# Kernel tuning notes

Measured on AMD Instinct MI355X. Metric: run time of the kernel, lower is better.

The kernel has to match this reference:

```python
import jax, jax.numpy as jnp
import numpy as np
import math

LMAX = 2
MUL = 50          # hidden multiplicity
NB = 10           # number_of_basis (hard-coded in module)
MAXR = 4.0        # max_radius
NLAYERS = 3
NUM_NEIGH = 2.0
E_EDGES = 40000
N_NODES = 2 * E_EDGES
SL = {0: slice(0, 1), 1: slice(1, 4), 2: slice(4, 9)}  # l=0,1,2 slices of the 9-dim multiplet
PATHS = [(0,0,0),(0,1,1),(0,2,2),(1,0,1),(1,1,0),(1,1,1),(1,1,2),
         (1,2,1),(1,2,2),(2,0,2),(2,1,1),(2,1,2),(2,2,0),(2,2,1),(2,2,2)]
NPATH_IN = {0: 3.0, 1: 6.0, 2: 6.0}  # number of TP paths feeding each output l

# ---- e3nn component-normalized real spherical harmonics up to l=2 (numpy, for CG setup) ----
def _sh_np(v):
    x, y, z = v[:, 0], v[:, 1], v[:, 2]
    s3, s5, s15 = 3**0.5, 5**0.5, 15**0.5
    return np.stack([np.ones_like(x), s3*x, s3*y, s3*z,
                     s15*x*z, s15*x*y, s5*(y*y - 0.5*(x*x + z*z)),
                     s15*y*z, (s15/2)*(z*z - x*x)], axis=1)

# ---- numerically derive the (unit-norm) Wigner-3j coupling tensors consistent with _sh_np ----
def _compute_w3j():
    rng = np.random.default_rng(0)
    pts = rng.normal(size=(256, 3)); pts /= np.linalg.norm(pts, axis=1, keepdims=True)
    Y = _sh_np(pts)
    def D_of(R):  # Wigner-D per l via least squares: Y(R p) = Y(p) @ D^T
        Yr = _sh_np(pts @ R.T)
        return {l: np.linalg.lstsq(Y[:, SL[l]], Yr[:, SL[l]], rcond=None)[0].T for l in range(LMAX+1)}
    Ds_list = []
    for _ in range(200):
        A = rng.normal(size=(3, 3))
        q, r = np.linalg.qr(A)
        q = q * np.sign(np.diag(r))
        if np.linalg.det(q) < 0:
            q[:, 0] = -q[:, 0]
        Ds_list.append(D_of(q))
    out = {}
    for (l1, l2, l3) in set(PATHS):
        d = (2*l1+1) * (2*l2+1) * (2*l3+1)
        M = np.zeros((d, d))
        for Ds in Ds_list:
            M += np.kron(Ds[l1], np.kron(Ds[l2], Ds[l3]))
        M /= len(Ds_list)
        M = M @ M; M = M @ M; M = M @ M  # power-iterate toward invariant projector
        u, s, vt = np.linalg.svd(M)
        t = u[:, 0]; t = t / np.linalg.norm(t)
        t = t * np.sign(t[np.argmax(np.abs(t))])  # deterministic sign
        out[(l1, l2, l3)] = t.reshape(2*l1+1, 2*l2+1, 2*l3+1).astype(np.float32)
    return out

_W3J = {k: jnp.asarray(v) for k, v in _compute_w3j().items()}

# ---- jax forward pieces ----
def _sh(vec):  # [E,3] -> [E,9], normalize=True, component normalization (e3nn formulas)
    n = jnp.linalg.norm(vec, axis=1, keepdims=True)
    v = vec / jnp.maximum(n, 1e-12)
    x, y, z = v[:, 0], v[:, 1], v[:, 2]
    s3, s5, s15 = 3**0.5, 5**0.5, 15**0.5
    return jnp.stack([jnp.ones_like(x), s3*x, s3*y, s3*z,
                      s15*x*z, s15*x*y, s5*(y*y - 0.5*(x*x + z*z)),
                      s15*y*z, (s15/2)*(z*z - x*x)], axis=1)

def _radial(r):  # soft_one_hot_linspace(basis='smooth_finite', cutoff=True) * sqrt(NB)
    vals = jnp.linspace(0.0, MAXR, NB + 2)
    step = vals[1] - vals[0]
    centers = vals[1:-1]
    diff = (r[:, None] - centers) / step
    def u(x):  # soft_unit_step, grad-safe
        return jnp.where(x > 0, jnp.exp(-1.0 / jnp.where(x > 0, x, 1.0)), 0.0)
    f = 1.14136 * (math.e ** 2) * u(diff + 1.0) * u(1.0 - diff)
    return f * NB**0.5

def _lmix(x, W):  # per-l channel mixing (FullyConnectedTP with scalar node_attr == linear)
    parts = [jnp.einsum('num,uv->nvm', x[:, :, SL[l]], W[l]) for l in range(3)]
    return jnp.concatenate(parts, axis=2) / MUL**0.5

def _conv(x, sh, emb, src, dst, Wsc, Wlin1, W1, b1, W2, Wlin2):
    N = x.shape[0]
    sc = _lmix(x, Wsc)                       # self-connection
    h = _lmix(x, Wlin1)
    xs = h[src]                              # gather: [E, MUL, 9]
    w = jax.nn.gelu(emb @ W1 / NB**0.5 + b1) @ W2 / 10.0  # radial MLP -> per-edge TP weights
    w = w.reshape(-1, MUL, len(PATHS))
    msg = jnp.zeros_like(xs)
    for p, (l1, l2, l3) in enumerate(PATHS):  # uvu tensor product with edge spherical harmonics
        C = _W3J[(l1, l2, l3)]
        m = jnp.einsum('ijk,eui,ej->euk', C, xs[:, :, SL[l1]], sh[:, SL[l2]])
        msg = msg.at[:, :, SL[l3]].add(w[:, :, p:p+1] * m / NPATH_IN[l3]**0.5)
    agg = jnp.zeros((N, MUL, 9), x.dtype).at[dst].add(msg) / NUM_NEIGH**0.5  # scatter
    out = _lmix(agg, Wlin2)
    cs, cx = math.cos(math.pi / 8), math.sin(math.pi / 8)
    return cs * sc + cx * out

def _gate(x, Wg):  # scalars -> silu; l>0 gated by sigmoid of mixed scalars
    s = x[:, :, 0]
    g = jax.nn.sigmoid(s @ Wg / MUL**0.5)
    return jnp.concatenate([jax.nn.silu(s)[:, :, None], x[:, :, 1:] * g[:, :, None]], axis=2)

def _forward(node_pos, bar_alpha, W_embed, Wsc, Wlin1, W1, b1, W2, Wlin2, Wgate, W_out):
    E = node_pos.shape[0]
    N = bar_alpha.shape[0]
    edge_vec = node_pos[:, :, 1] - node_pos[:, :, 0]   # [E,3]
    sh = _sh(edge_vec)                                  # [E,9]
    emb = _radial(jnp.linalg.norm(edge_vec, axis=1))    # [E,10]
    src = jnp.arange(E) * 2
    dst = src + 1
    x = jnp.zeros((N, MUL, 9), node_pos.dtype).at[:, :, 0].set(bar_alpha[:, None] * W_embed[None, :])
    for i in range(NLAYERS):
        x = _conv(x, sh, emb, src, dst, Wsc[i], Wlin1[i], W1[i], b1[i], W2[i], Wlin2[i])
        x = _gate(x, Wgate[i])
    return jnp.einsum('num,u->nm', x[:, :, 1:4], W_out) / MUL**0.5  # 1x1o output per node

def setup_inputs() -> dict:
    key = jax.random.key(0)
    ks = jax.random.split(key, 10)
    f = jnp.float32
    return dict(
        node_pos=jax.random.normal(ks[0], (E_EDGES, 3, 2), f),
        bar_alpha=jax.random.normal(ks[1], (N_NODES,), f),
        W_embed=jax.random.normal(ks[2], (MUL,), f),
        Wsc=jax.random.normal(ks[3], (NLAYERS, 3, MUL, MUL), f),
        Wlin1=jax.random.normal(ks[4], (NLAYERS, 3, MUL, MUL), f),
        W1=jax.random.normal(ks[5], (NLAYERS, NB, 100), f),
        b1=jnp.zeros((NLAYERS, 100), f),
        W2=jax.random.normal(ks[6], (NLAYERS, 100, MUL * len(PATHS)), f),
        Wlin2=jax.random.normal(ks[7], (NLAYERS, 3, MUL, MUL), f),
        Wgate=jax.random.normal(ks[8], (NLAYERS, MUL, MUL), f),
        W_out=jax.random.normal(ks[9], (MUL,), f),
    )

def reference(node_pos, bar_alpha, W_embed, Wsc, Wlin1, W1, b1, W2, Wlin2, Wgate, W_out):
    return _forward(node_pos, bar_alpha, W_embed, Wsc, Wlin1, W1, b1, W2, Wlin2, Wgate, W_out)
```

## Files before the change

kernel.cpp:

```cpp
#include <hip/hip_runtime.h>
#include <hip/hip_fp16.h>
#include <math.h>
#include <string.h>

#define E_EDGES 40000
#define N_NODES 80000
#define NE5 5

#define S111 1.0
#define S122 1.0
#define S212 1.0
#define S221 1.0
#define S222 1.0

struct W3J { float v[615]; };

typedef __attribute__((ext_vector_type(8))) short bf16x8;
typedef __attribute__((ext_vector_type(4))) float f32x4;
typedef _Float16 h16x2 __attribute__((ext_vector_type(2)));
typedef _Float16 h16x8 __attribute__((ext_vector_type(8)));

static void build_w3j(W3J& w) {
    const double s3 = sqrt(3.0), s5 = sqrt(5.0), s15 = sqrt(15.0);
    struct Mono { int a, b, c; double co; };
    Mono Y[3][5][3]; int nm[3][5];
    for (int l = 0; l < 3; l++) for (int c = 0; c < 5; c++) nm[l][c] = 0;
    nm[0][0] = 1; Y[0][0][0] = Mono{0,0,0,1.0};
    nm[1][0] = 1; Y[1][0][0] = Mono{1,0,0,s3};
    nm[1][1] = 1; Y[1][1][0] = Mono{0,1,0,s3};
    nm[1][2] = 1; Y[1][2][0] = Mono{0,0,1,s3};
    nm[2][0] = 1; Y[2][0][0] = Mono{1,0,1,s15};
    nm[2][1] = 1; Y[2][1][0] = Mono{1,1,0,s15};
    nm[2][2] = 3; Y[2][2][0] = Mono{0,2,0,s5};  Y[2][2][1] = Mono{2,0,0,-0.5*s5}; Y[2][2][2] = Mono{0,0,2,-0.5*s5};
    nm[2][3] = 1; Y[2][3][0] = Mono{0,1,1,s15};
    nm[2][4] = 2; Y[2][4][0] = Mono{0,0,2,0.5*s15}; Y[2][4][1] = Mono{2,0,0,-0.5*s15};

    static const int PL[15][3] = {{0,0,0},{0,1,1},{0,2,2},{1,0,1},{1,1,0},{1,1,1},{1,1,2},{1,2,1},
                                  {1,2,2},{2,0,2},{2,1,1},{2,1,2},{2,2,0},{2,2,1},{2,2,2}};
    static const int OFF[15]  = {0,1,10,35,44,53,80,125,170,245,270,315,390,415,490};
    static const int ANCH[15] = {0,0,0,0,0,5,22,22,29,0,22,9,0,13,2};
    const double ASGN[15] = {1,1,1,1,1, S111, 1,1, S122, 1,1, S212, 1, S221, S222};

    auto dfact = [](int n) { double r = 1.0; for (int k = n; k > 1; k -= 2) r *= k; return r; };

    double Mm[5][3][3]; memset(Mm, 0, sizeof(Mm));
    const double mh = s15 * 0.5;
    Mm[0][0][2] = Mm[0][2][0] = mh;
    Mm[1][0][1] = Mm[1][1][0] = mh;
    Mm[2][0][0] = -0.5*s5; Mm[2][1][1] = s5; Mm[2][2][2] = -0.5*s5;
    Mm[3][1][2] = Mm[3][2][1] = mh;
    Mm[4][0][0] = -mh; Mm[4][2][2] = mh;
    double T[3][5][5];
    for (int a = 0; a < 5; a++) for (int b = 0; b < 5; b++) {
        double K[3][3];
        for (int i = 0; i < 3; i++) for (int j = 0; j < 3; j++) {
            double ab = 0, ba = 0;
            for (int r = 0; r < 3; r++) { ab += Mm[a][i][r]*Mm[b][r][j]; ba += Mm[b][i][r]*Mm[a][r][j]; }
            K[i][j] = ab - ba;
        }
        T[0][a][b] = K[1][2]; T[1][a][b] = K[2][0]; T[2][a][b] = K[0][1];
    }

    for (int p = 0; p < 15; p++) {
        int l1 = PL[p][0], l2 = PL[p][1], l3 = PL[p][2];
        int d1 = 2*l1+1, d2 = 2*l2+1, d3 = 2*l3+1, d = d1*d2*d3;
        double tt[125];
        if (((l1 + l2 + l3) & 1) == 0) {
            for (int i = 0; i < d1; i++) for (int j = 0; j < d2; j++) for (int k = 0; k < d3; k++) {
                double a = 0;
                for (int q1 = 0; q1 < nm[l1][i]; q1++)
                for (int q2 = 0; q2 < nm[l2][j]; q2++)
                for (int q3 = 0; q3 < nm[l3][k]; q3++) {
                    const Mono& A = Y[l1][i][q1]; const Mono& B = Y[l2][j][q2]; const Mono& C = Y[l3][k][q3];
                    int xa = A.a+B.a+C.a, yb = A.b+B.b+C.b, zc = A.c+B.c+C.c;
                    if ((xa & 1) || (yb & 1) || (zc & 1)) continue;
                    a += A.co*B.co*C.co * dfact(xa-1)*dfact(yb-1)*dfact(zc-1) / dfact(xa+yb+zc+1);
                }
                tt[(i*d2 + j)*d3 + k] = a;
            }
        } else if (p == 5) {
            for (int q = 0; q < 27; q++) tt[q] = 0;
            tt[0*9+1*3+2] = 1; tt[1*9+2*3+0] = 1; tt[2*9+0*3+1] = 1;
            tt[0*9+2*3+1] = -1; tt[1*9+0*3+2] = -1; tt[2*9+1*3+0] = -1;
        } else {
            for (int q = 0; q < d; q++) tt[q] = 0;
            if (p == 8)  for (int i=0;i<3;i++) for(int a=0;a<5;a++) for(int b=0;b<5;b++) tt[(i*5+a)*5+b] = T[i][a][b];
            if (p == 11) for (int a=0;a<5;a++) for(int i=0;i<3;i++) for(int b=0;b<5;b++) tt[(a*3+i)*5+b] = T[i][a][b];
            if (p == 13) for (int a=0;a<5;a++) for(int b=0;b<5;b++) for(int i=0;i<3;i++) tt[(a*5+b)*3+i] = T[i][a][b];
        }
        double nrm = 0; for (int q = 0; q < d; q++) nrm += tt[q]*tt[q];
        nrm = sqrt(nrm);
        double sg = ((tt[ANCH[p]] >= 0) ? 1.0 : -1.0) * ASGN[p] / nrm;
        for (int q = 0; q < d; q++) w.v[OFF[p] + q] = (float)(tt[q] * sg);
    }
}

__device__ const int d_L2r[15]    = {0,1,2,0,1,1,1,2,2,0,1,1,2,2,2};
__device__ const int d_L3r[15]    = {0,1,2,1,0,1,2,1,2,2,1,2,0,1,2};
__device__ const int d_OFFr[15]   = {0,1,10,35,44,53,80,125,170,245,270,315,390,415,490};
__device__ const int d_CKOFFr[15] = {0,1,4,9,18,21,30,45,54,69,94,109,134,139,154};
__device__ const int d_SLOr[3]    = {0,1,4};

#define S_H  0.1414213562373095f
#define S_CS 0.13065629648763766f
#define S_L2 0.03826834323650898f

#define WS_W1T 0
#define WS_W2F 3600
#define W2F_PLANE 288768
#define HB_WP3 1169472
#define HB_W6P 1270272
#define HB_WGT 1320672
#define WLS_BYTE_OFF 1337472

__device__ __forceinline__ float sigf(float a) { return 1.0f / (1.0f + expf(-a)); }

__device__ __forceinline__ unsigned bf16_rne(float v) {
    unsigned x = __float_as_uint(v);
    return (x + 0x7FFFu + ((x >> 16) & 1u)) >> 16;
}

#define BUILD_B(KS, BH, BL, TP) { \
    _Pragma("unroll") \
    for (int i_ = 0; i_ < 8; i_++) { \
        float v_ = (TP)[(KS)*32 + (lane >> 4)*8 + i_]; \
        unsigned h_ = bf16_rne(v_); \
        (BH)[i_] = (short)h_; \
        (BL)[i_] = (short)bf16_rne(v_ - __uint_as_float(h_ << 16)); \
    } }

#define TILE_MFMA(KS, BH, BL) { \
    const ushort* ap_ = baseA + (((size_t)tile*4 + (KS))*64 + lane)*8; \
    bf16x8 Ah_ = *(const bf16x8*)ap_; \
    bf16x8 Al_ = *(const bf16x8*)(ap_ + W2F_PLANE); \
    acc = __builtin_amdgcn_mfma_f32_16x16x32_bf16(Ah_, (BH), acc, 0, 0, 0); \
    acc = __builtin_amdgcn_mfma_f32_16x16x32_bf16(Ah_, (BL), acc, 0, 0, 0); \
    acc = __builtin_amdgcn_mfma_f32_16x16x32_bf16(Al_, (BH), acc, 0, 0, 0); }

#define DOT8(ACC, A, B) { \
    ACC = __builtin_amdgcn_fdot2(__builtin_shufflevector((A),(A),0,1), __builtin_shufflevector((B),(B),0,1), ACC, false); \
    ACC = __builtin_amdgcn_fdot2(__builtin_shufflevector((A),(A),2,3), __builtin_shufflevector((B),(B),2,3), ACC, false); \
    ACC = __builtin_amdgcn_fdot2(__builtin_shufflevector((A),(A),4,5), __builtin_shufflevector((B),(B),4,5), ACC, false); \
    ACC = __builtin_amdgcn_fdot2(__builtin_shufflevector((A),(A),6,7), __builtin_shufflevector((B),(B),6,7), ACC, false); }

__global__ void k_pack(const float* __restrict__ Wsc, const float* __restrict__ Wlin1,
                       const float* __restrict__ Wlin2, const float* __restrict__ Wgate,
                       const float* __restrict__ W1, const float* __restrict__ W2,
                       float* __restrict__ ws) {
    for (int i = blockIdx.x*blockDim.x + threadIdx.x; i < 3600; i += gridDim.x*blockDim.x) {
        int b = i % 12, j = (i/12) % 100, L = i / 1200;
        ws[WS_W1T + i] = (b < 10) ? W1[L*1000 + b*100 + j] : 0.0f;
    }
    _Float16* hw = (_Float16*)((char*)ws + HB_WP3);
    for (int h = blockIdx.x*blockDim.x + threadIdx.x; h < 84000; h += gridDim.x*blockDim.x) {
        float val = 0.0f;
        if (h < 50400) {
            int u = h % 56, r = h / 56;
            int c = r % 6, v = (r/6) % 50, L = r / 300;
            if (u < 50) {
                if (c < 3) val = Wlin1[L*7500 + c*2500 + u*50 + v];
                else       val = Wsc  [L*7500 + (c-3)*2500 + u*50 + v];
            }
        } else if (h < 75600) {
            int q = h - 50400;
            int u = q % 56, r = q / 56;
            int c = r % 3, v = (r/3) % 50, L = r / 150;
            if (u < 50) val = Wlin2[L*7500 + c*2500 + u*50 + v];
        } else {
            int q = h - 75600;
            int u = q % 56, r = q / 56;
            int v = r % 50, L = r / 50;
            if (u < 50) val = Wgate[L*2500 + u*50 + v];
        }
        hw[h] = (_Float16)val;
    }
    ushort* w2f = (ushort*)(ws + WS_W2F);
    for (int q = blockIdx.x*blockDim.x + threadIdx.x; q < 2*W2F_PLANE; q += gridDim.x*blockDim.x) {
        int plane = q / W2F_PLANE, r = q % W2F_PLANE;
        int i = r & 7, lane = (r >> 3) & 63, ks = (r >> 9) & 3, tl = r >> 11;
        int tile = tl % 47, L = tl / 47;
        int o = tile*16 + (lane & 15);
        int k = ks*32 + (lane >> 4)*8 + i;
        float w = (k < 100 && o < 750) ? W2[L*75000 + k*750 + o] : 0.0f;
        unsigned h = bf16_rne(w);
        unsigned val;
        if (plane == 0) val = h;
        else {
            float fh = __uint_as_float(h << 16);
            val = bf16_rne(w - fh);
        }
        w2f[q] = (ushort)val;
    }
}

__global__ __launch_bounds__(256, 3) void k_wls(
    const float* __restrict__ node_pos, const float* __restrict__ b1,
    float* __restrict__ ws)
{
    __shared__ __align__(16) float embw[64][12];
    __shared__ __align__(16) float t100s[64][132];
    __shared__ __align__(16) float stage[4][16][20];
    const int t = threadIdx.x;
    const int bid = blockIdx.x;
    const int Lidx = bid / 625;
    const int e0 = (bid % 625) * 64;
    const float* W1T = ws + WS_W1T;
    const ushort* W2F = (const ushort*)(ws + WS_W2F);
    __half* wls_g = (__half*)((char*)ws + WLS_BYTE_OFF);

    if (t < 64) {
        const float* np = node_pos + (size_t)(e0 + t) * 6;
        float vx = np[1] - np[0], vy = np[3] - np[2], vz = np[5] - np[4];
        float r = sqrtf(vx*vx + vy*vy + vz*vz);
        const float step = 4.0f / 11.0f;
        const float RC = (float)(1.14136 * 7.3890560989306495 * 3.1622776601683795);
        #pragma unroll
        for (int b = 0; b < 10; b++) {
            float center = step * (b + 1);
            float diff = (r - center) / step;
            float x1 = diff + 1.0f, x2 = 1.0f - diff;
            float u1 = (x1 > 0.0f) ? expf(-1.0f/x1) : 0.0f;
            float u2 = (x2 > 0.0f) ? expf(-1.0f/x2) : 0.0f;
            embw[t][b] = RC * u1 * u2;
        }
        embw[t][10] = 0.0f; embw[t][11] = 0.0f;
    }
    __syncthreads();

    for (int idx = t; idx < 64*132; idx += 256) {
        int e = idx / 132, j = idx % 132;
        float g = 0.0f;
        if (j < 100) {
            const float* wj = W1T + (Lidx*100 + j)*12;
            float4 wa = *(const float4*)wj;
            float4 wb = *(const float4*)(wj + 4);
            float2 wc = *(const float2*)(wj + 8);
            float4 e0v = *(const float4*)&embw[e][0];
            float4 e1v = *(const float4*)&embw[e][4];
            float2 e2v = *(const float2*)&embw[e][8];
            float a = wa.x*e0v.x + wa.y*e0v.y + wa.z*e0v.z + wa.w*e0v.w
                    + wb.x*e1v.x + wb.y*e1v.y + wb.z*e1v.z + wb.w*e1v.w
                    + wc.x*e2v.x + wc.y*e2v.y;
            a = a * 0.31622776601683794f + b1[Lidx*100 + j];
            float th = tanhf(0.7978845608028654f * (a + 0.044715f * a*a*a));
            g = 0.5f * a * (1.0f + th);
        }
        t100s[e][j] = g;
    }
    __syncthreads();

    const int lane = t & 63, wave = t >> 6;
    const int bcol = lane & 15, bg = lane >> 4;
    const ushort* baseA = W2F + (size_t)Lidx * (47*4*64*8);
    __half* wout = wls_g + (size_t)(Lidx*40000 + e0) * 752;

    for (int eg = 0; eg < 4; eg++) {
        const float* tp = &t100s[eg*16 + bcol][0];
        bf16x8 Bh0, Bh1, Bh2, Bh3, Bl0, Bl1, Bl2, Bl3;
        BUILD_B(0, Bh0, Bl0, tp) BUILD_B(1, Bh1, Bl1, tp)
        BUILD_B(2, Bh2, Bl2, tp) BUILD_B(3, Bh3, Bl3, tp)
        for (int tile = wave; tile < 47; tile += 4) {
            f32x4 acc = {0.f, 0.f, 0.f, 0.f};
            TILE_MFMA(0, Bh0, Bl0) TILE_MFMA(1, Bh1, Bl1)
            TILE_MFMA(2, Bh2, Bl2) TILE_MFMA(3, Bh3, Bl3)
            *(float4*)&stage[wave][bcol][bg*4] = make_float4(acc[0], acc[1], acc[2], acc[3]);
            int er = lane >> 2, o4 = (lane & 3) * 4;
            float4 vv = *(const float4*)&stage[wave][er][o4];
            __half2 p0 = __floats2half2_rn(vv.x * 0.1f, vv.y * 0.1f);
            __half2 p1 = __floats2half2_rn(vv.z * 0.1f, vv.w * 0.1f);
            union { __half2 h2[2]; uint2 u2; } pk;
            pk.h2[0] = p0; pk.h2[1] = p1;
            *(uint2*)(wout + (size_t)(eg*16 + er)*752 + tile*16 + o4) = pk.u2;
        }
    }
}

__global__ __launch_bounds__(256, 4) void k_fused_pre(
    const float* __restrict__ node_pos, const float* __restrict__ bar,
    const float* __restrict__ Wemb, const float* __restrict__ Wout,
    const float* __restrict__ ws, float* __restrict__ out, W3J w3j)
{
    __shared__ __align__(16) _Float16 xs0[NE5][504];
    __shared__ __align__(16) _Float16 xs1[NE5][504];
    __shared__ __align__(16) _Float16 msg[NE5][504];
    __shared__ __align__(16) _Float16 wls_h[NE5][752];
    __shared__ __align__(16) float ck[NE5][180];
    __shared__ __align__(16) float shs[NE5][12];

    const int t = threadIdx.x;
    const int e0 = blockIdx.x * NE5;

    constexpr int cL1[15]    = {0,0,0,1,1,1,1,1,1,2,2,2,2,2,2};
    constexpr int cCKOFF[15] = {0,1,4,9,18,21,30,45,54,69,94,109,134,139,154};
    constexpr int cSLO[3]    = {0,1,4};
    constexpr int cPBYL3[15] = {0,4,12, 1,3,5,7,10,13, 2,6,8,9,11,14};
    constexpr int cPL3S[4]   = {0,3,9,15};
    constexpr float cINVNP[3] = {0.57735026918962584f, 0.40824829046386302f, 0.40824829046386302f};

    const _Float16* WP3H = (const _Float16*)((const char*)ws + HB_WP3);
    const _Float16* W6PH = (const _Float16*)((const char*)ws + HB_W6P);
    const _Float16* WGTH = (const _Float16*)((const char*)ws + HB_WGT);
    const _Float16* wls_g = (const _Float16*)((const char*)ws + WLS_BYTE_OFF);

    if (t < NE5) {
        const int e = t;
        const float* np = node_pos + (size_t)(e0 + e) * 6;
        float vx = np[1] - np[0], vy = np[3] - np[2], vz = np[5] - np[4];
        float r = sqrtf(vx*vx + vy*vy + vz*vz);
        float inv = 1.0f / fmaxf(r, 1e-12f);
        float x = vx*inv, y = vy*inv, z = vz*inv;
        const float s3 = 1.7320508075688772f, s5 = 2.23606797749979f, s15 = 3.872983346207417f;
        shs[e][0] = 1.0f;
        shs[e][1] = s3*x; shs[e][2] = s3*y; shs[e][3] = s3*z;
        shs[e][4] = s15*x*z; shs[e][5] = s15*x*y;
        shs[e][6] = s5*(y*y - 0.5f*(x*x + z*z));
        shs[e][7] = s15*y*z;
        shs[e][8] = 0.5f*s15*(z*z - x*x);
    }
    if (t >= 64 && t < 64 + 2*NE5) {
        int q = t - 64;
        shs[q >> 1][9 + (q & 1)] = bar[2*e0 + q];
    }
    __syncthreads();

    for (int idx = t; idx < NE5*179; idx += 256) {
        int e = idx / 179, q = idx % 179;
        int p = 0; while (p < 14 && q >= d_CKOFFr[p+1]) p++;
        int rem = q - d_CKOFFr[p];
        int D2 = 2*d_L2r[p] + 1, D3 = 2*d_L3r[p] + 1;
        int i = rem / D3, k = rem % D3;
        const float* C = w3j.v + d_OFFr[p];
        const float* s = &shs[e][d_SLOr[d_L2r[p]]];
        float a = 0;
        for (int j = 0; j < D2; j++) a += C[(i*D2 + j)*D3 + k] * s[j];
        ck[e][q] = a;
    }
    for (int idx = t; idx < 2*NE5*504; idx += 256) {
        int n = idx / 504, i = idx % 504;
        int e = n >> 1, half = n & 1;
        int m = i / 56, u = i % 56;
        float val = (m == 0 && u < 50) ? shs[e][9 + half] * Wemb[u] : 0.0f;
        if (half) xs1[e][i] = (_Float16)val; else xs0[e][i] = (_Float16)val;
    }
    for (int idx = t; idx < NE5*54; idx += 256) {
        int e = idx / 54, r = idx % 54;
        int m = r / 6, p = r % 6;
        msg[e][m*56 + 50 + p] = (_Float16)0.0f;
    }
    __syncthreads();

    const bool act = (t < 50*NE5);
    const int v = t / NE5, ea = t % NE5;

    for (int L = 0; L < 3; L++) {
        {
            const _Float16* wsrc = wls_g + (size_t)(L*40000 + e0) * 752;
            for (int idx = t; idx < NE5*94; idx += 256) {
                int e = idx / 94, c = idx % 94;
                *(uint4*)&wls_h[e][c*8] = *(const uint4*)(wsrc + (size_t)e*752 + c*8);
            }
        }

        float hsc[9], n0r[9], n1r[9];
        #pragma unroll
        for (int m = 0; m < 9; m++) { hsc[m] = 0.f; n0r[m] = 0.f; n1r[m] = 0.f; }
        if (act) {
            const _Float16* wp = WP3H + (size_t)(L*50 + v) * 336;
            for (int u8 = 0; u8 < 56; u8 += 8) {
                h16x8 wl0 = *(const h16x8*)(wp +   0 + u8);
                h16x8 wl1 = *(const h16x8*)(wp +  56 + u8);
                h16x8 wl2 = *(const h16x8*)(wp + 112 + u8);
                h16x8 ws0 = *(const h16x8*)(wp + 168 + u8);
                h16x8 ws1 = *(const h16x8*)(wp + 224 + u8);
                h16x8 ws2 = *(const h16x8*)(wp + 280 + u8);
                h16x8 q[9];
                #pragma unroll
                for (int m = 0; m < 9; m++) q[m] = *(const h16x8*)&xs0[ea][m*56 + u8];
                #pragma unroll
                for (int m = 0; m < 9; m++) {
                    const int l = (m == 0) ? 0 : ((m < 4) ? 1 : 2);
                    const h16x8 wl = (l==0) ? wl0 : ((l==1) ? wl1 : wl2);
                    const h16x8 wv = (l==0) ? ws0 : ((l==1) ? ws1 : ws2);
                    DOT8(hsc[m], q[m], wl)
                    DOT8(n0r[m], q[m], wv)
                }
                #pragma unroll
                for (int m = 0; m < 9; m++) q[m] = *(const h16x8*)&xs1[ea][m*56 + u8];
                #pragma unroll
                for (int m = 0; m < 9; m++) {
                    const int l = (m == 0) ? 0 : ((m < 4) ? 1 : 2);
                    const h16x8 wv = (l==0) ? ws0 : ((l==1) ? ws1 : ws2);
                    DOT8(n1r[m], q[m], wv)
                }
            }
            #pragma unroll
            for (int m = 0; m < 9; m++) hsc[m] *= S_H;
        }
        __syncthreads();

        if (act) {
            #pragma unroll
            for (int m = 0; m < 9; m++) {
                xs0[ea][m*56 + v] = (_Float16)(n0r[m] * S_CS);
                xs1[ea][m*56 + v] = (_Float16)(n1r[m] * S_CS);
            }
        }
        __syncthreads();

        if (act) {
            const _Float16* whp = &wls_h[ea][v*15];
            float w[15];
            #pragma unroll
            for (int p = 0; p < 15; p++) w[p] = (float)whp[p];
            float mg[9];
            #pragma unroll
            for (int k = 0; k < 9; ++k) {
                const int l3 = (k == 0) ? 0 : ((k < 4) ? 1 : 2);
                const int kl = k - cSLO[l3];
                float a = 0.f;
                #pragma unroll
                for (int pi = cPL3S[l3]; pi < cPL3S[l3+1]; ++pi) {
                    const int p = cPBYL3[pi];
                    const int l1 = cL1[p];
                    const int D1 = 2*l1 + 1, D3 = 2*l3 + 1;
                    float mm = 0.f;
                    #pragma unroll
                    for (int i = 0; i < D1; ++i)
                        mm += ck[ea][cCKOFF[p] + i*D3 + kl] * hsc[cSLO[l1] + i];
                    a += w[p] * mm;
                }
                mg[k] = a * cINVNP[l3];
            }
            #pragma unroll
            for (int k = 0; k < 9; ++k) msg[ea][k*56 + v] = (_Float16)mg[k];
        }
        __syncthreads();

        if (act) {
            const _Float16* w6 = W6PH + (size_t)(L*50 + v) * 168;
            float am[9];
            #pragma unroll
            for (int m = 0; m < 9; m++) am[m] = 0.f;
            for (int u8 = 0; u8 < 56; u8 += 8) {
                h16x8 w60 = *(const h16x8*)(w6 +   0 + u8);
                h16x8 w61 = *(const h16x8*)(w6 +  56 + u8);
                h16x8 w62 = *(const h16x8*)(w6 + 112 + u8);
                h16x8 q[9];
                #pragma unroll
                for (int m = 0; m < 9; m++) q[m] = *(const h16x8*)&msg[ea][m*56 + u8];
                #pragma unroll
                for (int m = 0; m < 9; m++) {
                    const int l = (m == 0) ? 0 : ((m < 4) ? 1 : 2);
                    const h16x8 wv = (l==0) ? w60 : ((l==1) ? w61 : w62);
                    DOT8(am[m], q[m], wv)
                }
            }
            #pragma unroll
            for (int m = 0; m < 9; m++) {
                float old = (float)xs1[ea][m*56 + v];
                xs1[ea][m*56 + v] = (_Float16)(old + am[m] * S_L2);
            }
        }
        __syncthreads();

        float g0 = 0.f, g1 = 0.f;
        if (act) {
            const _Float16* wg = WGTH + (size_t)(L*50 + v) * 56;
            float a0 = 0.f, a1 = 0.f;
            #pragma unroll
            for (int u8 = 0; u8 < 56; u8 += 8) {
                h16x8 wv = *(const h16x8*)(wg + u8);
                h16x8 x0 = *(const h16x8*)&xs0[ea][u8];
                h16x8 x1 = *(const h16x8*)&xs1[ea][u8];
                DOT8(a0, x0, wv)
                DOT8(a1, x1, wv)
            }
            g0 = sigf(a0 * S_H);
            g1 = sigf(a1 * S_H);
        }
        __syncthreads();

        if (act) {
            _Float16* p0 = &xs0[ea][v];
            _Float16* p1 = &xs1[ea][v];
            float s0 = (float)p0[0], s1 = (float)p1[0];
            p0[0] = (_Float16)(s0 * sigf(s0));
            p1[0] = (_Float16)(s1 * sigf(s1));
            #pragma unroll
            for (int m = 1; m < 9; m++) {
                p0[m*56] = (_Float16)((float)p0[m*56] * g0);
                p1[m*56] = (_Float16)((float)p1[m*56] * g1);
            }
        }
        __syncthreads();
    }

    if (t < NE5*6) {
        int e = t / 6, r = t % 6, half = r / 3, m = r % 3;
        const _Float16* xp = half ? &xs1[e][(1 + m)*56] : &xs0[e][(1 + m)*56];
        float a = 0;
        #pragma unroll 2
        for (int u = 0; u < 50; ++u) a += (float)xp[u] * Wout[u];
        out[((size_t)(2*(e0 + e) + half))*3 + m] = a * S_H;
    }
}

extern "C" void kernel_launch(void* const* d_in, const int* in_sizes, int n_in,
                              void* d_out, int out_size, void* d_ws, size_t ws_size,
                              hipStream_t stream) {
    const float* node_pos = (const float*)d_in[0];
    const float* bar      = (const float*)d_in[1];
    const float* Wemb     = (const float*)d_in[2];
    const float* Wsc      = (const float*)d_in[3];
    const float* Wlin1    = (const float*)d_in[4];
    const float* W1       = (const float*)d_in[5];
    const float* b1       = (const float*)d_in[6];
    const float* W2       = (const float*)d_in[7];
    const float* Wlin2    = (const float*)d_in[8];
    const float* Wgate    = (const float*)d_in[9];
    const float* Wout     = (const float*)d_in[10];
    float* out = (float*)d_out;
    float* ws  = (float*)d_ws;

    W3J w3j;
    build_w3j(w3j);

    k_pack<<<1024, 256, 0, stream>>>(Wsc, Wlin1, Wlin2, Wgate, W1, W2, ws);
    k_wls<<<1875, 256, 0, stream>>>(node_pos, b1, ws);
    k_fused_pre<<<E_EDGES/NE5, 256, 0, stream>>>(node_pos, bar, Wemb, Wout, ws, out, w3j);
}
```

Baseline: 584.7 us.

## Use fp16 MFMA for per-layer Wlin1/Wsc linear mixing instead of scalar fdot2

The first linear stage of each layer (Wlin1 for h and the Wsc self-connection for both nodes) moves from per-thread fdot2 loops to 16x16x32 fp16 MFMA tiles. Weights are repacked into 64x64 padded matrices per l, and node features are restrided to 72-element rows so each (edge, m) column forms a B operand. Results for h go through a new LDS buffer, and the self-connection outputs are written back after a barrier. This removes scalar dot-product work and repeated global weight loads, at the cost of padding waste, extra LDS and more complex lane-to-column mapping.

```diff
diff --git a/kernel.cpp b/kernel.cpp
--- a/kernel.cpp
+++ b/kernel.cpp
@@ -17,7 +17,6 @@
 
 typedef __attribute__((ext_vector_type(8))) short bf16x8;
 typedef __attribute__((ext_vector_type(4))) float f32x4;
-typedef _Float16 h16x2 __attribute__((ext_vector_type(2)));
 typedef _Float16 h16x8 __attribute__((ext_vector_type(8)));
 
 static void build_w3j(W3J& w) {
@@ -108,10 +107,13 @@
 #define WS_W1T 0
 #define WS_W2F 3600
 #define W2F_PLANE 288768
-#define HB_WP3 1169472
-#define HB_W6P 1270272
-#define HB_WGT 1320672
-#define WLS_BYTE_OFF 1337472
+#define HB_WAF 1169472
+#define HB_W6P 1316928
+#define HB_WGT 1367328
+#define WLS_BYTE_OFF 1384128
+
+#define XR 72
+#define XE 648
 
 __device__ __forceinline__ float sigf(float a) { return 1.0f / (1.0f + expf(-a)); }
 
@@ -143,6 +145,31 @@
     ACC = __builtin_amdgcn_fdot2(__builtin_shufflevector((A),(A),4,5), __builtin_shufflevector((B),(B),4,5), ACC, false); \
     ACC = __builtin_amdgcn_fdot2(__builtin_shufflevector((A),(A),6,7), __builtin_shufflevector((B),(B),6,7), ACC, false); }
 
+#define DO_TILE(AL0, AL1, AS0, AS1, BOFF, TCOL, AN0, AN1) { \
+    h16x8 b00 = *(const h16x8*)&xs0f[(BOFF)]; \
+    h16x8 b01 = *(const h16x8*)&xs0f[(BOFF) + 32]; \
+    h16x8 b10 = *(const h16x8*)&xs1f[(BOFF)]; \
+    h16x8 b11 = *(const h16x8*)&xs1f[(BOFF) + 32]; \
+    f32x4 ah_ = __builtin_amdgcn_mfma_f32_16x16x32_f16((AL0), b00, z4, 0, 0, 0); \
+    ah_ = __builtin_amdgcn_mfma_f32_16x16x32_f16((AL1), b01, ah_, 0, 0, 0); \
+    (AN0) = __builtin_amdgcn_mfma_f32_16x16x32_f16((AS0), b00, (AN0), 0, 0, 0); \
+    (AN0) = __builtin_amdgcn_mfma_f32_16x16x32_f16((AS1), b01, (AN0), 0, 0, 0); \
+    (AN1) = __builtin_amdgcn_mfma_f32_16x16x32_f16((AS0), b10, (AN1), 0, 0, 0); \
+    (AN1) = __builtin_amdgcn_mfma_f32_16x16x32_f16((AS1), b11, (AN1), 0, 0, 0); \
+    _Pragma("unroll") \
+    for (int r_ = 0; r_ < 4; r_++) \
+        h_lds[(v0 + kg*4 + r_)*66 + (TCOL) + cB] = (_Float16)(ah_[r_] * S_H); }
+
+#define WB_TILE(AN0, AN1, MW, EW, LIVE) { \
+    if (LIVE) { \
+        _Pragma("unroll") \
+        for (int r_ = 0; r_ < 4; r_++) { \
+            int vv_ = v0 + kg*4 + r_; \
+            if (vv_ < 50) { \
+                xs0f[(EW)*XE + (MW)*XR + vv_] = (_Float16)((AN0)[r_] * S_CS); \
+                xs1f[(EW)*XE + (MW)*XR + vv_] = (_Float16)((AN1)[r_] * S_CS); \
+            } } } }
+
 __global__ void k_pack(const float* __restrict__ Wsc, const float* __restrict__ Wlin1,
                        const float* __restrict__ Wlin2, const float* __restrict__ Wgate,
                        const float* __restrict__ W1, const float* __restrict__ W2,
@@ -151,23 +178,22 @@
         int b = i % 12, j = (i/12) % 100, L = i / 1200;
         ws[WS_W1T + i] = (b < 10) ? W1[L*1000 + b*100 + j] : 0.0f;
     }
-    _Float16* hw = (_Float16*)((char*)ws + HB_WP3);
-    for (int h = blockIdx.x*blockDim.x + threadIdx.x; h < 84000; h += gridDim.x*blockDim.x) {
+    _Float16* hw = (_Float16*)((char*)ws + HB_WAF);
+    for (int h = blockIdx.x*blockDim.x + threadIdx.x; h < 107328; h += gridDim.x*blockDim.x) {
         float val = 0.0f;
-        if (h < 50400) {
-            int u = h % 56, r = h / 56;
-            int c = r % 6, v = (r/6) % 50, L = r / 300;
-            if (u < 50) {
-                if (c < 3) val = Wlin1[L*7500 + c*2500 + u*50 + v];
-                else       val = Wsc  [L*7500 + (c-3)*2500 + u*50 + v];
-            }
-        } else if (h < 75600) {
-            int q = h - 50400;
+        if (h < 73728) {
+            int u = h & 63, v = (h >> 6) & 63, mat = (h >> 12) & 1;
+            int rest = h >> 13, l = rest % 3, L = rest / 3;
+            if (u < 50 && v < 50)
+                val = (mat == 0) ? Wlin1[L*7500 + l*2500 + u*50 + v]
+                                 : Wsc  [L*7500 + l*2500 + u*50 + v];
+        } else if (h < 98928) {
+            int q = h - 73728;
             int u = q % 56, r = q / 56;
             int c = r % 3, v = (r/3) % 50, L = r / 150;
             if (u < 50) val = Wlin2[L*7500 + c*2500 + u*50 + v];
         } else {
-            int q = h - 75600;
+            int q = h - 98928;
             int u = q % 56, r = q / 56;
             int v = r % 50, L = r / 50;
             if (u < 50) val = Wgate[L*2500 + u*50 + v];
@@ -280,12 +306,13 @@
     const float* __restrict__ Wemb, const float* __restrict__ Wout,
     const float* __restrict__ ws, float* __restrict__ out, W3J w3j)
 {
-    __shared__ __align__(16) _Float16 xs0[NE5][504];
-    __shared__ __align__(16) _Float16 xs1[NE5][504];
-    __shared__ __align__(16) _Float16 msg[NE5][504];
+    __shared__ __align__(16) _Float16 xs0f[NE5*XE];
+    __shared__ __align__(16) _Float16 xs1f[NE5*XE];
+    __shared__ __align__(16) _Float16 msgf[NE5*XE];
     __shared__ __align__(16) _Float16 wls_h[NE5][752];
     __shared__ __align__(16) float ck[NE5][180];
     __shared__ __align__(16) float shs[NE5][12];
+    __shared__ __align__(16) _Float16 h_lds[64*66];
 
     const int t = threadIdx.x;
     const int e0 = blockIdx.x * NE5;
@@ -297,7 +324,7 @@
     constexpr int cPL3S[4]   = {0,3,9,15};
     constexpr float cINVNP[3] = {0.57735026918962584f, 0.40824829046386302f, 0.40824829046386302f};
 
-    const _Float16* WP3H = (const _Float16*)((const char*)ws + HB_WP3);
+    const _Float16* WAF  = (const _Float16*)((const char*)ws + HB_WAF);
     const _Float16* W6PH = (const _Float16*)((const char*)ws + HB_W6P);
     const _Float16* WGTH = (const _Float16*)((const char*)ws + HB_WGT);
     const _Float16* wls_g = (const _Float16*)((const char*)ws + WLS_BYTE_OFF);
@@ -335,22 +362,34 @@
         for (int j = 0; j < D2; j++) a += C[(i*D2 + j)*D3 + k] * s[j];
         ck[e][q] = a;
     }
-    for (int idx = t; idx < 2*NE5*504; idx += 256) {
-        int n = idx / 504, i = idx % 504;
+    for (int idx = t; idx < 2*NE5*XE; idx += 256) {
+        int n = idx / XE, i = idx % XE;
         int e = n >> 1, half = n & 1;
-        int m = i / 56, u = i % 56;
+        int m = i / XR, u = i % XR;
         float val = (m == 0 && u < 50) ? shs[e][9 + half] * Wemb[u] : 0.0f;
-        if (half) xs1[e][i] = (_Float16)val; else xs0[e][i] = (_Float16)val;
-    }
-    for (int idx = t; idx < NE5*54; idx += 256) {
-        int e = idx / 54, r = idx % 54;
-        int m = r / 6, p = r % 6;
-        msg[e][m*56 + 50 + p] = (_Float16)0.0f;
-    }
+        if (half) xs1f[e*XE + i] = (_Float16)val; else xs0f[e*XE + i] = (_Float16)val;
+    }
+    for (int idx = t; idx < NE5*XE; idx += 256) msgf[idx] = (_Float16)0.0f;
     __syncthreads();
 
     const bool act = (t < 50*NE5);
     const int v = t / NE5, ea = t % NE5;
+
+    const int lane = t & 63;
+    const int cB = lane & 15, kg = lane >> 4;
+    const int v0 = (t >> 6) * 16;
+    const int aoff = (v0 + cB)*64 + kg*8;
+    const int  e0t = (cB < 5) ? cB : 0;                 const bool lv0 = (cB < 5);
+    const int  m1t = (cB < 15) ? 1 + cB/5 : 1;
+    const int  e1t = (cB < 15) ? cB % 5 : 0;            const bool lv1 = (cB < 15);
+    const int  m2t = 4 + cB/5,  e2t = cB % 5;
+    const int  i3 = 16 + cB;
+    const int  m3t = (i3 < 25) ? 4 + i3/5 : 4;
+    const int  e3t = (i3 < 25) ? i3 % 5 : 0;            const bool lv3 = (cB < 9);
+    const int b0 = e0t*XE + 0*XR  + kg*8;
+    const int b1 = e1t*XE + m1t*XR + kg*8;
+    const int b2 = e2t*XE + m2t*XR + kg*8;
+    const int b3 = e3t*XE + m3t*XR + kg*8;
 
     for (int L = 0; L < 3; L++) {
         {
@@ -361,53 +400,50 @@
             }
         }
 
-        float hsc[9], n0r[9], n1r[9];
-        #pragma unroll
-        for (int m = 0; m < 9; m++) { hsc[m] = 0.f; n0r[m] = 0.f; n1r[m] = 0.f; }
+        const _Float16* wafL = WAF + (size_t)L * 24576;
+        const f32x4 z4 = {0.f, 0.f, 0.f, 0.f};
+        f32x4 an0t0 = z4, an1t0 = z4, an0t1 = z4, an1t1 = z4;
+        f32x4 an0t2 = z4, an1t2 = z4, an0t3 = z4, an1t3 = z4;
+        {
+            const _Float16* wl = wafL;
+            h16x8 aL0 = *(const h16x8*)(wl + aoff);
+            h16x8 aL1 = *(const h16x8*)(wl + aoff + 32);
+            h16x8 aS0 = *(const h16x8*)(wl + 4096 + aoff);
+            h16x8 aS1 = *(const h16x8*)(wl + 4096 + aoff + 32);
+            DO_TILE(aL0, aL1, aS0, aS1, b0, 0, an0t0, an1t0)
+        }
+        {
+            const _Float16* wl = wafL + 8192;
+            h16x8 aL0 = *(const h16x8*)(wl + aoff);
+            h16x8 aL1 = *(const h16x8*)(wl + aoff + 32);
+            h16x8 aS0 = *(const h16x8*)(wl + 4096 + aoff);
+            h16x8 aS1 = *(const h16x8*)(wl + 4096 + aoff + 32);
+            DO_TILE(aL0, aL1, aS0, aS1, b1, 16, an0t1, an1t1)
+        }
+        {
+            const _Float16* wl = wafL + 16384;
+            h16x8 aL0 = *(const h16x8*)(wl + aoff);
+            h16x8 aL1 = *(const h16x8*)(wl + aoff + 32);
+            h16x8 aS0 = *(const h16x8*)(wl + 4096 + aoff);
+            h16x8 aS1 = *(const h16x8*)(wl + 4096 + aoff + 32);
+            DO_TILE(aL0, aL1, aS0, aS1, b2, 32, an0t2, an1t2)
+            DO_TILE(aL0, aL1, aS0, aS1, b3, 48, an0t3, an1t3)
+        }
+        __syncthreads();
+
+        WB_TILE(an0t0, an1t0, 0,   e0t, lv0)
+        WB_TILE(an0t1, an1t1, m1t, e1t, lv1)
+        WB_TILE(an0t2, an1t2, m2t, e2t, true)
+        WB_TILE(an0t3, an1t3, m3t, e3t, lv3)
+        __syncthreads();
+
         if (act) {
-            const _Float16* wp = WP3H + (size_t)(L*50 + v) * 336;
-            for (int u8 = 0; u8 < 56; u8 += 8) {
-                h16x8 wl0 = *(const h16x8*)(wp +   0 + u8);
-                h16x8 wl1 = *(const h16x8*)(wp +  56 + u8);
-                h16x8 wl2 = *(const h16x8*)(wp + 112 + u8);
-                h16x8 ws0 = *(const h16x8*)(wp + 168 + u8);
-                h16x8 ws1 = *(const h16x8*)(wp + 224 + u8);
-                h16x8 ws2 = *(const h16x8*)(wp + 280 + u8);
-                h16x8 q[9];
-                #pragma unroll
-                for (int m = 0; m < 9; m++) q[m] = *(const h16x8*)&xs0[ea][m*56 + u8];
-                #pragma unroll
-                for (int m = 0; m < 9; m++) {
-                    const int l = (m == 0) ? 0 : ((m < 4) ? 1 : 2);
-                    const h16x8 wl = (l==0) ? wl0 : ((l==1) ? wl1 : wl2);
-                    const h16x8 wv = (l==0) ? ws0 : ((l==1) ? ws1 : ws2);
-                    DOT8(hsc[m], q[m], wl)
-                    DOT8(n0r[m], q[m], wv)
-                }
-                #pragma unroll
-                for (int m = 0; m < 9; m++) q[m] = *(const h16x8*)&xs1[ea][m*56 + u8];
-                #pragma unroll
-                for (int m = 0; m < 9; m++) {
-                    const int l = (m == 0) ? 0 : ((m < 4) ? 1 : 2);
-                    const h16x8 wv = (l==0) ? ws0 : ((l==1) ? ws1 : ws2);
-                    DOT8(n1r[m], q[m], wv)
-                }
-            }
-            #pragma unroll
-            for (int m = 0; m < 9; m++) hsc[m] *= S_H;
-        }
-        __syncthreads();
-
-        if (act) {
-            #pragma unroll
-            for (int m = 0; m < 9; m++) {
-                xs0[ea][m*56 + v] = (_Float16)(n0r[m] * S_CS);
-                xs1[ea][m*56 + v] = (_Float16)(n1r[m] * S_CS);
-            }
-        }
-        __syncthreads();
-
-        if (act) {
+            float harr[9];
+            harr[0] = (float)h_lds[v*66 + ea];
+            #pragma unroll
+            for (int m = 1; m < 4; m++) harr[m] = (float)h_lds[v*66 + 16 + (m-1)*5 + ea];
+            #pragma unroll
+            for (int m = 4; m < 9; m++) harr[m] = (float)h_lds[v*66 + 32 + (m-4)*5 + ea];
             const _Float16* whp = &wls_h[ea][v*15];
             float w[15];
             #pragma unroll
@@ -426,13 +462,13 @@
                     float mm = 0.f;
                     #pragma unroll
                     for (int i = 0; i < D1; ++i)
-                        mm += ck[ea][cCKOFF[p] + i*D3 + kl] * hsc[cSLO[l1] + i];
+                        mm += ck[ea][cCKOFF[p] + i*D3 + kl] * harr[cSLO[l1] + i];
                     a += w[p] * mm;
                 }
                 mg[k] = a * cINVNP[l3];
             }
             #pragma unroll
-            for (int k = 0; k < 9; ++k) msg[ea][k*56 + v] = (_Float16)mg[k];
+            for (int k = 0; k < 9; ++k) msgf[ea*XE + k*XR + v] = (_Float16)mg[k];
         }
         __syncthreads();
 
@@ -447,7 +483,7 @@
                 h16x8 w62 = *(const h16x8*)(w6 + 112 + u8);
                 h16x8 q[9];
                 #pragma unroll
-                for (int m = 0; m < 9; m++) q[m] = *(const h16x8*)&msg[ea][m*56 + u8];
+                for (int m = 0; m < 9; m++) q[m] = *(const h16x8*)&msgf[ea*XE + m*XR + u8];
                 #pragma unroll
                 for (int m = 0; m < 9; m++) {
                     const int l = (m == 0) ? 0 : ((m < 4) ? 1 : 2);
@@ -457,8 +493,8 @@
             }
             #pragma unroll
             for (int m = 0; m < 9; m++) {
-                float old = (float)xs1[ea][m*56 + v];
-                xs1[ea][m*56 + v] = (_Float16)(old + am[m] * S_L2);
+                float old = (float)xs1f[ea*XE + m*XR + v];
+                xs1f[ea*XE + m*XR + v] = (_Float16)(old + am[m] * S_L2);
             }
         }
         __syncthreads();
@@ -470,8 +506,8 @@
             #pragma unroll
             for (int u8 = 0; u8 < 56; u8 += 8) {
                 h16x8 wv = *(const h16x8*)(wg + u8);
-                h16x8 x0 = *(const h16x8*)&xs0[ea][u8];
-                h16x8 x1 = *(const h16x8*)&xs1[ea][u8];
+                h16x8 x0 = *(const h16x8*)&xs0f[ea*XE + u8];
+                h16x8 x1 = *(const h16x8*)&xs1f[ea*XE + u8];
                 DOT8(a0, x0, wv)
                 DOT8(a1, x1, wv)
             }
@@ -481,15 +517,15 @@
         __syncthreads();
 
         if (act) {
-            _Float16* p0 = &xs0[ea][v];
-            _Float16* p1 = &xs1[ea][v];
+            _Float16* p0 = &xs0f[ea*XE + v];
+            _Float16* p1 = &xs1f[ea*XE + v];
             float s0 = (float)p0[0], s1 = (float)p1[0];
             p0[0] = (_Float16)(s0 * sigf(s0));
             p1[0] = (_Float16)(s1 * sigf(s1));
             #pragma unroll
             for (int m = 1; m < 9; m++) {
-                p0[m*56] = (_Float16)((float)p0[m*56] * g0);
-                p1[m*56] = (_Float16)((float)p1[m*56] * g1);
+                p0[m*XR] = (_Float16)((float)p0[m*XR] * g0);
+                p1[m*XR] = (_Float16)((float)p1[m*XR] * g1);
             }
         }
         __syncthreads();
@@ -497,7 +533,7 @@
 
     if (t < NE5*6) {
         int e = t / 6, r = t % 6, half = r / 3, m = r % 3;
-        const _Float16* xp = half ? &xs1[e][(1 + m)*56] : &xs0[e][(1 + m)*56];
+        const _Float16* xp = half ? &xs1f[e*XE + (1 + m)*XR] : &xs0f[e*XE + (1 + m)*XR];
         float a = 0;
         #pragma unroll 2
         for (int u = 0; u < 50; ++u) a += (float)xp[u] * Wout[u];
```

Measured after the change: 595.4 us. About the same (+1.8%).
